# Performance work log

Measured on AMD Instinct MI355X. Metric: run time of the kernel, lower is better.

Reference implementation:

```python
import jax, jax.numpy as jnp
import numpy as np

E = 1024      # embed_dim
H = 16        # num_heads
DH = E // H   # head_dim
CD = 512      # context_dim
S = 2048      # source length
B = 16        # batch
SCALE = DH ** -0.5


def setup_inputs() -> dict:
    key0 = jax.random.key(0)
    ks = jax.random.split(key0, 12)
    inp = {
        "query": jax.random.normal(ks[0], (1, B, E), jnp.float32),
        "key": jax.random.normal(ks[1], (S, B, E), jnp.float32),
        "value": jax.random.normal(ks[2], (S, B, E), jnp.float32),
        "context": jax.random.normal(ks[3], (B, CD), jnp.float32),
        # packed QKV input projection: [3E, E] (rows 0:E -> Q, E:2E -> K, 2E:3E -> V)
        "in_proj_weight": jax.random.normal(ks[4], (3 * E, E), jnp.float32) * 0.02,
        "in_proj_bias": jnp.zeros((3 * E,), jnp.float32),
        # context_layer: Linear(context_dim + embed_dim, embed_dim)
        "ctx_weight": jax.random.normal(ks[5], (E, CD + E), jnp.float32) * 0.02,
        "ctx_bias": jnp.zeros((E,), jnp.float32),
        # out_proj: Linear(E, E)
        "out_weight": jax.random.normal(ks[6], (E, E), jnp.float32) * 0.02,
        "out_bias": jnp.zeros((E,), jnp.float32),
        # bias_k / bias_v: learned extra KV position, shape [1,1,E] in torch
        "bias_k": jax.random.normal(ks[7], (E,), jnp.float32) * 0.02,
        "bias_v": jax.random.normal(ks[8], (E,), jnp.float32) * 0.02,
    }
    return inp


def _attention(query, key, value, context, in_proj_weight, in_proj_bias,
               ctx_weight, ctx_bias, out_weight, out_bias, bias_k, bias_v):
    tgt_len, bsz, _ = query.shape  # tgt_len == 1 (context cat requires it)
    # separate q/k/v input projections (slices of packed weight)
    q = query @ in_proj_weight[:E].T + in_proj_bias[:E]
    k = key @ in_proj_weight[E:2 * E].T + in_proj_bias[E:2 * E]
    v = value @ in_proj_weight[2 * E:].T + in_proj_bias[2 * E:]
    # context injection: concat context along feature dim, project back to E
    ctx_q = context[None]                                # [1, B, CD]
    ctx_k = jnp.broadcast_to(context[None], (k.shape[0], bsz, CD))
    q = jnp.concatenate([ctx_q, q], axis=-1) @ ctx_weight.T + ctx_bias
    k = jnp.concatenate([ctx_k, k], axis=-1) @ ctx_weight.T + ctx_bias
    q = q * SCALE
    # bias_k / bias_v appended as extra source position
    k = jnp.concatenate([k, jnp.broadcast_to(bias_k, (1, bsz, E))], axis=0)
    v = jnp.concatenate([v, jnp.broadcast_to(bias_v, (1, bsz, E))], axis=0)
    src_len = k.shape[0]
    # [L, B, E] -> [B*H, L, DH]
    qh = q.reshape(tgt_len, bsz * H, DH).transpose(1, 0, 2)
    kh = k.reshape(src_len, bsz * H, DH).transpose(1, 0, 2)
    vh = v.reshape(src_len, bsz * H, DH).transpose(1, 0, 2)
    scores = jnp.einsum("btd,bsd->bts", qh, kh)          # [B*H, T, S+1]
    weights = jax.nn.softmax(scores, axis=-1)
    attn = jnp.einsum("bts,bsd->btd", weights, vh)       # [B*H, T, DH]
    attn = attn.transpose(1, 0, 2).reshape(tgt_len, bsz, E)
    attn = attn @ out_weight.T + out_bias
    avg_weights = weights.reshape(bsz, H, tgt_len, src_len).sum(axis=1) / H
    return attn, avg_weights


def reference(query, key, value, context, in_proj_weight, in_proj_bias,
              ctx_weight, ctx_bias, out_weight, out_bias, bias_k, bias_v):
    return _attention(query, key, value, context, in_proj_weight, in_proj_bias,
                      ctx_weight, ctx_bias, out_weight, out_bias, bias_k, bias_v)
```

## Files before the change

### kernel.cpp

```cpp
#include <hip/hip_runtime.h>
#include <math.h>

#define E   1024
#define H   16
#define DH  64
#define CD  512
#define S   2048
#define B   16
#define SRC (S + 1)
#define SPAD 2052
#define SCALE 0.125f

#define OFF_CTXP 0
#define OFF_Q0   16384
#define OFF_BKP  32768
#define OFF_Q1S  33792
#define OFF_CK   50176
#define OFF_TT   66560
#define OFF_C0   328704
#define OFF_GP   328960
#define OFF_SC   1377536
#define OFF_WT   1902848
#define OFF_UP   2427392
#define OFF_U    6621696
#define OFF_AP   6883840

__global__ __launch_bounds__(256) void k_pre1(
    const float* __restrict__ query, const float* __restrict__ context,
    const float* __restrict__ ipw, const float* __restrict__ ipb,
    const float* __restrict__ cw, const float* __restrict__ cb,
    float* __restrict__ ws)
{
    int b  = blockIdx.x >> 6;
    int et = blockIdx.x & 63;
    int grp = threadIdx.x >> 4, l = threadIdx.x & 15;
    int e = et * 16 + grp;
    const float* crow = cw + (size_t)e * (CD + E);
    const float* ctx  = context + b * CD;
    float a1 = 0.f;
    #pragma unroll
    for (int c = l * 4; c < CD; c += 64) {
        float4 w4 = *(const float4*)(crow + c);
        float4 x4 = *(const float4*)(ctx + c);
        a1 += w4.x*x4.x + w4.y*x4.y + w4.z*x4.z + w4.w*x4.w;
    }
    const float* qrow = query + b * E;
    const float* wrow = ipw + (size_t)e * E;
    float a2 = 0.f;
    #pragma unroll
    for (int f = l * 4; f < E; f += 64) {
        float4 w4 = *(const float4*)(wrow + f);
        float4 x4 = *(const float4*)(qrow + f);
        a2 += w4.x*x4.x + w4.y*x4.y + w4.z*x4.z + w4.w*x4.w;
    }
    float a3 = 0.f;
    if (b == 0) {
        const float* c2 = crow + CD;
        const float* bk = ipb + E;
        #pragma unroll
        for (int f = l * 4; f < E; f += 64) {
            float4 w4 = *(const float4*)(c2 + f);
            float4 x4 = *(const float4*)(bk + f);
            a3 += w4.x*x4.x + w4.y*x4.y + w4.z*x4.z + w4.w*x4.w;
        }
    }
    #pragma unroll
    for (int m = 8; m >= 1; m >>= 1) {
        a1 += __shfl_xor(a1, m, 64);
        a2 += __shfl_xor(a2, m, 64);
        a3 += __shfl_xor(a3, m, 64);
    }
    if (l == 0) {
        ws[OFF_CTXP + b*E + e] = a1 + cb[e];
        ws[OFF_Q0   + b*E + e] = a2 + ipb[e];
        if (b == 0) ws[OFF_BKP + e] = a3;
    }
}

__global__ __launch_bounds__(256) void k_pre2(
    const float* __restrict__ cw, float* __restrict__ ws)
{
    int b  = blockIdx.x >> 6;
    int et = blockIdx.x & 63;
    int grp = threadIdx.x >> 4, l = threadIdx.x & 15;
    int e = et * 16 + grp;
    const float* q0 = ws + OFF_Q0 + b*E;
    const float* c2row = cw + (size_t)e * (CD + E) + CD;
    float acc = 0.f;
    #pragma unroll
    for (int f = l * 4; f < E; f += 64) {
        float4 w4 = *(const float4*)(c2row + f);
        float4 x4 = *(const float4*)(q0 + f);
        acc += w4.x*x4.x + w4.y*x4.y + w4.z*x4.z + w4.w*x4.w;
    }
    #pragma unroll
    for (int m = 8; m >= 1; m >>= 1) acc += __shfl_xor(acc, m, 64);
    if (l == 0) {
        float ctxp = ws[OFF_CTXP + b*E + e];
        ws[OFF_Q1S + b*E + e] = (ctxp + acc) * SCALE;
        ws[OFF_CK  + b*E + e] = ctxp + ws[OFF_BKP + e];
    }
}

__global__ __launch_bounds__(256) void k_pre3(
    const float* __restrict__ cw, float* __restrict__ ws)
{
    int bh = blockIdx.x >> 2;
    int f  = ((blockIdx.x & 3) << 8) + threadIdx.x;
    int b = bh >> 4, h = bh & 15;
    const float* q1 = ws + OFF_Q1S + b*E + h*DH;
    float acc = 0.f;
    #pragma unroll 8
    for (int d = 0; d < DH; ++d)
        acc += q1[d] * cw[(size_t)(h*DH + d)*(CD+E) + CD + f];
    ws[OFF_TT + f*256 + bh] = acc;
}

__global__ __launch_bounds__(256) void k_pre3b(
    const float* __restrict__ bias_k, float* __restrict__ ws)
{
    int bh = threadIdx.x;
    int b = bh >> 4, h = bh & 15;
    const float* q1 = ws + OFF_Q1S + b*E + h*DH;
    const float* ck = ws + OFF_CK  + b*E + h*DH;
    const float* bk = bias_k + h*DH;
    float c0 = 0.f, sb = 0.f;
    for (int d = 0; d < DH; ++d) { float q = q1[d]; c0 += q*ck[d]; sb += q*bk[d]; }
    ws[OFF_C0 + bh] = c0;
    ws[OFF_SC + (size_t)bh*SPAD + S] = sb;
}

__global__ __launch_bounds__(256) void k_g(
    const float* __restrict__ ipw, float* __restrict__ ws)
{
    int kc = blockIdx.x >> 7;
    int nt = (blockIdx.x >> 5) & 3;
    int mt = blockIdx.x & 31;
    int n  = (nt << 8) + threadIdx.x;
    int m0 = mt << 3;
    int f0 = kc << 8;
    const float* tT = ws + OFF_TT;
    const float* wk = ipw + (size_t)E * E;
    float acc[8];
    #pragma unroll
    for (int m = 0; m < 8; ++m) acc[m] = 0.f;
    #pragma unroll 4
    for (int f = f0; f < f0 + 256; ++f) {
        float wv = wk[(size_t)f*E + n];
        const float* tr = tT + f*256 + m0;
        #pragma unroll
        for (int m = 0; m < 8; ++m) acc[m] += tr[m] * wv;
    }
    float* gp = ws + OFF_GP + (size_t)kc * (256*E);
    #pragma unroll
    for (int m = 0; m < 8; ++m) gp[(size_t)(m0+m)*E + n] = acc[m];
}

__global__ __launch_bounds__(256) void k_gsum(float* __restrict__ ws)
{
    int id = blockIdx.x * 256 + threadIdx.x;
    float a = ws[OFF_GP + id]
            + ws[OFF_GP + 1*(256*E) + id]
            + ws[OFF_GP + 2*(256*E) + id]
            + ws[OFF_GP + 3*(256*E) + id];
    ws[OFF_GP + id] = a;
}

__global__ __launch_bounds__(512, 2) void k_scores(
    const float* __restrict__ key, float* __restrict__ ws)
{
    __shared__ float lds[8704];
    int b  = blockIdx.x >> 5;
    int sc = blockIdx.x & 31;
    int tid = threadIdx.x;
    int w = __builtin_amdgcn_readfirstlane(tid >> 6);
    int l = tid & 63;
    int r = sc*64 + l;
    const float* kbase = key + (((size_t)r*B + b) << 10) + w*128;
    const float* gbase = ws + OFF_GP + (size_t)b*(16*1024) + w*128;
    float acc[16];
    #pragma unroll
    for (int h = 0; h < 16; ++h) acc[h] = 0.f;

    #pragma unroll 1
    for (int sub = 0; sub < 4; ++sub) {
        const float* kp = kbase + sub*32;
        float4 kk[8];
        #pragma unroll
        for (int j = 0; j < 8; ++j) kk[j] = *(const float4*)(kp + j*4);
        const float* gp0 = gbase + sub*32;
        #pragma unroll
        for (int h = 0; h < 16; ++h) {
            const float* gp = gp0 + h*1024;
            float a = 0.f;
            #pragma unroll
            for (int j = 0; j < 8; ++j) {
                float4 gv = *(const float4*)(gp + j*4);
                a += kk[j].x*gv.x + kk[j].y*gv.y + kk[j].z*gv.z + kk[j].w*gv.w;
            }
            acc[h] += a;
        }
    }

    float* pr = lds + (w*64 + l)*17;
    #pragma unroll
    for (int h = 0; h < 16; ++h) pr[h] = acc[h];
    __syncthreads();

    int l2 = tid & 63, pp = tid >> 6;
    #pragma unroll
    for (int k2 = 0; k2 < 2; ++k2) {
        int h = pp*2 + k2;
        float sum = 0.f;
        #pragma unroll
        for (int ww = 0; ww < 8; ++ww) sum += lds[(ww*64 + l2)*17 + h];
        int bh = b*16 + h;
        ws[OFF_SC + (size_t)bh*SPAD + sc*64 + l2] = sum + ws[OFF_C0 + bh];
    }
}

__global__ __launch_bounds__(256) void k_softmax(float* __restrict__ ws)
{
    int bh = blockIdx.x; int b = bh >> 4, h = bh & 15;
    int tid = threadIdx.x, lane = tid & 63, wid = tid >> 6;
    const float* row = ws + OFF_SC + (size_t)bh*SPAD;
    __shared__ float red[4];
    float v[9];
    float m = -1e30f;
    #pragma unroll
    for (int i = 0; i < 9; ++i) {
        int s = tid + (i << 8);
        if (s < SRC) { v[i] = row[s]; m = fmaxf(m, v[i]); } else v[i] = -1e30f;
    }
    #pragma unroll
    for (int k = 1; k < 64; k <<= 1) m = fmaxf(m, __shfl_xor(m, k, 64));
    if (lane == 0) red[wid] = m;
    __syncthreads();
    m = fmaxf(fmaxf(red[0], red[1]), fmaxf(red[2], red[3]));
    __syncthreads();
    float sum = 0.f;
    #pragma unroll
    for (int i = 0; i < 9; ++i) {
        int s = tid + (i << 8);
        if (s < SRC) { v[i] = expf(v[i] - m); sum += v[i]; }
    }
    #pragma unroll
    for (int k = 1; k < 64; k <<= 1) sum += __shfl_xor(sum, k, 64);
    if (lane == 0) red[wid] = sum;
    __syncthreads();
    sum = red[0] + red[1] + red[2] + red[3];
    float inv = 1.0f / sum;
    float* wt = ws + OFF_WT;
    #pragma unroll
    for (int i = 0; i < 9; ++i) {
        int s = tid + (i << 8);
        if (s < SRC) wt[((size_t)(b*SRC + s) << 4) + h] = v[i] * inv;
    }
}

__global__ __launch_bounds__(256) void k_avg(
    const float* __restrict__ ws, float* __restrict__ out)
{
    int id = blockIdx.x * 256 + threadIdx.x;
    if (id >= B * SRC) return;
    const float* p = ws + OFF_WT + (size_t)id * 16;
    float a = 0.f;
    #pragma unroll
    for (int j = 0; j < 16; j += 4) {
        float4 w4 = *(const float4*)(p + j);
        a += w4.x + w4.y + w4.z + w4.w;
    }
    out[B*E + id] = a * (1.0f / H);
}

__global__ __launch_bounds__(256) void k_u(
    const float* __restrict__ value, float* __restrict__ ws)
{
    int b  = blockIdx.x >> 5;
    int sc = (blockIdx.x >> 1) & 15;
    int fh = blockIdx.x & 1;
    int f  = (fh << 9) + threadIdx.x * 2;
    float2 acc[16];
    #pragma unroll
    for (int h = 0; h < 16; ++h) { acc[h].x = 0.f; acc[h].y = 0.f; }
    int s0 = sc << 7;
    for (int i = 0; i < 128; ++i) {
        int s = s0 + i;
        const float* wr = ws + OFF_WT + ((size_t)(b*SRC + s) << 4);
        float2 vv = *(const float2*)(value + (((size_t)s*B + b) << 10) + f);
        #pragma unroll
        for (int h = 0; h < 16; ++h) {
            float wv = wr[h];
            acc[h].x += wv * vv.x; acc[h].y += wv * vv.y;
        }
    }
    float* up = ws + OFF_UP + ((size_t)(sc*B + b) << 4) * E;
    #pragma unroll
    for (int h = 0; h < 16; ++h)
        *(float2*)(up + (size_t)h*E + f) = acc[h];
}

__global__ __launch_bounds__(256) void k_ured(float* __restrict__ ws)
{
    int id = blockIdx.x * 256 + threadIdx.x;
    float a = 0.f;
    #pragma unroll
    for (int c = 0; c < 16; ++c) a += ws[OFF_UP + (size_t)c*(B*H*E) + id];
    ws[OFF_U + id] = a;
}

__global__ __launch_bounds__(256) void k_attnpre(
    const float* __restrict__ ipw, const float* __restrict__ ipb,
    const float* __restrict__ bias_v, float* __restrict__ ws)
{
    int b  = blockIdx.x >> 6;
    int et = blockIdx.x & 63;
    int grp = threadIdx.x >> 4, l = threadIdx.x & 15;
    int e = et * 16 + grp;
    int h = e >> 6;
    const float* wvr = ipw + (size_t)(2*E + e) * E;
    const float* ur  = ws + OFF_U + (size_t)(b*16 + h) * E;
    float acc = 0.f;
    #pragma unroll
    for (int ff = l * 4; ff < E; ff += 64) {
        float4 w4 = *(const float4*)(wvr + ff);
        float4 u4 = *(const float4*)(ur + ff);
        acc += w4.x*u4.x + w4.y*u4.y + w4.z*u4.z + w4.w*u4.w;
    }
    #pragma unroll
    for (int m = 8; m >= 1; m >>= 1) acc += __shfl_xor(acc, m, 64);
    if (l == 0) {
        float wS = ws[OFF_WT + ((size_t)(b*SRC + S) << 4) + h];
        ws[OFF_AP + b*E + e] = acc + ipb[2*E + e] * (1.0f - wS) + wS * bias_v[e];
    }
}

__global__ __launch_bounds__(256) void k_out(
    const float* __restrict__ ow, const float* __restrict__ ob,
    const float* __restrict__ ws, float* __restrict__ out)
{
    int b  = blockIdx.x >> 6;
    int et = blockIdx.x & 63;
    int grp = threadIdx.x >> 4, l = threadIdx.x & 15;
    int o = et * 16 + grp;
    const float* wr = ow + (size_t)o * E;
    const float* ap = ws + OFF_AP + b*E;
    float acc = 0.f;
    #pragma unroll
    for (int e = l * 4; e < E; e += 64) {
        float4 w4 = *(const float4*)(wr + e);
        float4 a4 = *(const float4*)(ap + e);
        acc += w4.x*a4.x + w4.y*a4.y + w4.z*a4.z + w4.w*a4.w;
    }
    #pragma unroll
    for (int m = 8; m >= 1; m >>= 1) acc += __shfl_xor(acc, m, 64);
    if (l == 0) out[b*E + o] = acc + ob[o];
}

extern "C" void kernel_launch(void* const* d_in, const int* in_sizes, int n_in,
                              void* d_out, int out_size, void* d_ws, size_t ws_size,
                              hipStream_t stream)
{
    const float* query   = (const float*)d_in[0];
    const float* key     = (const float*)d_in[1];
    const float* value   = (const float*)d_in[2];
    const float* context = (const float*)d_in[3];
    const float* ipw     = (const float*)d_in[4];
    const float* ipb     = (const float*)d_in[5];
    const float* cw      = (const float*)d_in[6];
    const float* cb      = (const float*)d_in[7];
    const float* ow      = (const float*)d_in[8];
    const float* ob      = (const float*)d_in[9];
    const float* bias_k  = (const float*)d_in[10];
    const float* bias_v  = (const float*)d_in[11];
    float* out = (float*)d_out;
    float* ws  = (float*)d_ws;

    hipLaunchKernelGGL(k_pre1,    dim3(1024), dim3(256),  0, stream, query, context, ipw, ipb, cw, cb, ws);
    hipLaunchKernelGGL(k_pre2,    dim3(1024), dim3(256),  0, stream, cw, ws);
    hipLaunchKernelGGL(k_pre3,    dim3(1024), dim3(256),  0, stream, cw, ws);
    hipLaunchKernelGGL(k_pre3b,   dim3(1),    dim3(256),  0, stream, bias_k, ws);
    hipLaunchKernelGGL(k_g,       dim3(512),  dim3(256),  0, stream, ipw, ws);
    hipLaunchKernelGGL(k_gsum,    dim3(1024), dim3(256),  0, stream, ws);
    hipLaunchKernelGGL(k_scores,  dim3(512),  dim3(512),  0, stream, key, ws);
    hipLaunchKernelGGL(k_softmax, dim3(256),  dim3(256),  0, stream, ws);
    hipLaunchKernelGGL(k_avg,     dim3(129),  dim3(256),  0, stream, ws, out);
    hipLaunchKernelGGL(k_u,       dim3(512),  dim3(256),  0, stream, value, ws);
    hipLaunchKernelGGL(k_ured,    dim3(1024), dim3(256),  0, stream, ws);
    hipLaunchKernelGGL(k_attnpre, dim3(1024), dim3(256),  0, stream, ipw, ipb, bias_v, ws);
    hipLaunchKernelGGL(k_out,     dim3(1024), dim3(256),  0, stream, ow, ob, ws, out);
}
```

Baseline: 193.3 us.

## Transpose weight/T layouts, fold pre3b into scores, drop U reduction kernel

Switches the softmax-weight buffer from [b,s,h] to a per-head row layout [bh,s] and the T buffer to [bh,f], so writes are coalesced and pre3 uses float4 loads over fewer blocks. The tiny single-block pre3b kernel is removed: each scores block recomputes the c0 and bias_k terms in shared memory. k_u now processes 64 source rows per block with float4 values, and the separate 16-way reduction kernel is removed; k_attnpre instead loops over 32 partial U chunks, with the W_v row held in registers. This cuts two launches and improves access patterns, but attnpre now reads much more partial data and k_g reads T with a 1024 stride.

```diff
diff --git a/kernel.cpp b/kernel.cpp
--- a/kernel.cpp
+++ b/kernel.cpp
@@ -17,13 +17,11 @@
 #define OFF_Q1S  33792
 #define OFF_CK   50176
 #define OFF_TT   66560
-#define OFF_C0   328704
 #define OFF_GP   328960
 #define OFF_SC   1377536
 #define OFF_WT   1902848
 #define OFF_UP   2427392
-#define OFF_U    6621696
-#define OFF_AP   6883840
+#define OFF_AP   10816000
 
 __global__ __launch_bounds__(256) void k_pre1(
     const float* __restrict__ query, const float* __restrict__ context,
@@ -105,29 +103,18 @@
 __global__ __launch_bounds__(256) void k_pre3(
     const float* __restrict__ cw, float* __restrict__ ws)
 {
-    int bh = blockIdx.x >> 2;
-    int f  = ((blockIdx.x & 3) << 8) + threadIdx.x;
+    int bh = blockIdx.x;
     int b = bh >> 4, h = bh & 15;
+    int f = threadIdx.x * 4;
     const float* q1 = ws + OFF_Q1S + b*E + h*DH;
-    float acc = 0.f;
+    float4 a; a.x = a.y = a.z = a.w = 0.f;
     #pragma unroll 8
-    for (int d = 0; d < DH; ++d)
-        acc += q1[d] * cw[(size_t)(h*DH + d)*(CD+E) + CD + f];
-    ws[OFF_TT + f*256 + bh] = acc;
-}
-
-__global__ __launch_bounds__(256) void k_pre3b(
-    const float* __restrict__ bias_k, float* __restrict__ ws)
-{
-    int bh = threadIdx.x;
-    int b = bh >> 4, h = bh & 15;
-    const float* q1 = ws + OFF_Q1S + b*E + h*DH;
-    const float* ck = ws + OFF_CK  + b*E + h*DH;
-    const float* bk = bias_k + h*DH;
-    float c0 = 0.f, sb = 0.f;
-    for (int d = 0; d < DH; ++d) { float q = q1[d]; c0 += q*ck[d]; sb += q*bk[d]; }
-    ws[OFF_C0 + bh] = c0;
-    ws[OFF_SC + (size_t)bh*SPAD + S] = sb;
+    for (int d = 0; d < DH; ++d) {
+        float q = q1[d];
+        float4 w4 = *(const float4*)(cw + (size_t)(h*DH + d)*(CD+E) + CD + f);
+        a.x += q*w4.x; a.y += q*w4.y; a.z += q*w4.z; a.w += q*w4.w;
+    }
+    *(float4*)(ws + OFF_TT + (size_t)bh*1024 + f) = a;
 }
 
 __global__ __launch_bounds__(256) void k_g(
@@ -147,9 +134,9 @@
     #pragma unroll 4
     for (int f = f0; f < f0 + 256; ++f) {
         float wv = wk[(size_t)f*E + n];
-        const float* tr = tT + f*256 + m0;
-        #pragma unroll
-        for (int m = 0; m < 8; ++m) acc[m] += tr[m] * wv;
+        #pragma unroll
+        for (int m = 0; m < 8; ++m)
+            acc[m] += tT[(size_t)(m0+m)*1024 + f] * wv;
     }
     float* gp = ws + OFF_GP + (size_t)kc * (256*E);
     #pragma unroll
@@ -167,12 +154,28 @@
 }
 
 __global__ __launch_bounds__(512, 2) void k_scores(
-    const float* __restrict__ key, float* __restrict__ ws)
+    const float* __restrict__ key, const float* __restrict__ bias_k,
+    float* __restrict__ ws)
 {
     __shared__ float lds[8704];
+    __shared__ float exA[256];
+    __shared__ float exB[256];
     int b  = blockIdx.x >> 5;
     int sc = blockIdx.x & 31;
     int tid = threadIdx.x;
+
+    if (tid < 256) {
+        int h = tid >> 4, seg = tid & 15;
+        const float* q1 = ws + OFF_Q1S + b*E + h*DH + seg*4;
+        const float* ck = ws + OFF_CK  + b*E + h*DH + seg*4;
+        const float* bk = bias_k + h*DH + seg*4;
+        float4 q4 = *(const float4*)q1;
+        float4 c4 = *(const float4*)ck;
+        float4 b4 = *(const float4*)bk;
+        exA[tid] = q4.x*c4.x + q4.y*c4.y + q4.z*c4.z + q4.w*c4.w;
+        exB[tid] = q4.x*b4.x + q4.y*b4.y + q4.z*b4.z + q4.w*b4.w;
+    }
+
     int w = __builtin_amdgcn_readfirstlane(tid >> 6);
     int l = tid & 63;
     int r = sc*64 + l;
@@ -214,14 +217,23 @@
         float sum = 0.f;
         #pragma unroll
         for (int ww = 0; ww < 8; ++ww) sum += lds[(ww*64 + l2)*17 + h];
+        float c0 = 0.f;
+        #pragma unroll
+        for (int seg = 0; seg < 16; ++seg) c0 += exA[h*16 + seg];
         int bh = b*16 + h;
-        ws[OFF_SC + (size_t)bh*SPAD + sc*64 + l2] = sum + ws[OFF_C0 + bh];
+        ws[OFF_SC + (size_t)bh*SPAD + sc*64 + l2] = sum + c0;
+        if (sc == 0 && l2 == 0) {
+            float sb = 0.f;
+            #pragma unroll
+            for (int seg = 0; seg < 16; ++seg) sb += exB[h*16 + seg];
+            ws[OFF_SC + (size_t)bh*SPAD + S] = sb;
+        }
     }
 }
 
 __global__ __launch_bounds__(256) void k_softmax(float* __restrict__ ws)
 {
-    int bh = blockIdx.x; int b = bh >> 4, h = bh & 15;
+    int bh = blockIdx.x;
     int tid = threadIdx.x, lane = tid & 63, wid = tid >> 6;
     const float* row = ws + OFF_SC + (size_t)bh*SPAD;
     __shared__ float red[4];
@@ -250,63 +262,60 @@
     __syncthreads();
     sum = red[0] + red[1] + red[2] + red[3];
     float inv = 1.0f / sum;
-    float* wt = ws + OFF_WT;
+    float* wrow = ws + OFF_WT + (size_t)bh*SRC;
     #pragma unroll
     for (int i = 0; i < 9; ++i) {
         int s = tid + (i << 8);
-        if (s < SRC) wt[((size_t)(b*SRC + s) << 4) + h] = v[i] * inv;
+        if (s < SRC) wrow[s] = v[i] * inv;
     }
 }
 
 __global__ __launch_bounds__(256) void k_avg(
     const float* __restrict__ ws, float* __restrict__ out)
 {
-    int id = blockIdx.x * 256 + threadIdx.x;
-    if (id >= B * SRC) return;
-    const float* p = ws + OFF_WT + (size_t)id * 16;
+    int b = blockIdx.x / 9, i = blockIdx.x % 9;
+    int s = i*256 + threadIdx.x;
+    if (s >= SRC) return;
+    const float* p = ws + OFF_WT + (size_t)(b*16)*SRC + s;
     float a = 0.f;
     #pragma unroll
-    for (int j = 0; j < 16; j += 4) {
-        float4 w4 = *(const float4*)(p + j);
-        a += w4.x + w4.y + w4.z + w4.w;
-    }
-    out[B*E + id] = a * (1.0f / H);
+    for (int h = 0; h < 16; ++h) a += p[(size_t)h*SRC];
+    out[B*E + b*SRC + s] = a * (1.0f / H);
 }
 
 __global__ __launch_bounds__(256) void k_u(
     const float* __restrict__ value, float* __restrict__ ws)
 {
     int b  = blockIdx.x >> 5;
-    int sc = (blockIdx.x >> 1) & 15;
-    int fh = blockIdx.x & 1;
-    int f  = (fh << 9) + threadIdx.x * 2;
-    float2 acc[16];
-    #pragma unroll
-    for (int h = 0; h < 16; ++h) { acc[h].x = 0.f; acc[h].y = 0.f; }
-    int s0 = sc << 7;
-    for (int i = 0; i < 128; ++i) {
-        int s = s0 + i;
-        const float* wr = ws + OFF_WT + ((size_t)(b*SRC + s) << 4);
-        float2 vv = *(const float2*)(value + (((size_t)s*B + b) << 10) + f);
+    int sc = blockIdx.x & 31;
+    int f  = threadIdx.x * 4;
+    const float* wtb = ws + OFF_WT + (size_t)(b*16)*SRC;
+    float4 acc[16];
+    #pragma unroll
+    for (int h = 0; h < 16; ++h) { acc[h].x = acc[h].y = acc[h].z = acc[h].w = 0.f; }
+    int s0 = sc * 64;
+    #pragma unroll 1
+    for (int sub = 0; sub < 8; ++sub) {
+        int ss = s0 + sub*8;
+        float4 vv[8];
+        #pragma unroll
+        for (int j = 0; j < 8; ++j)
+            vv[j] = *(const float4*)(value + (((size_t)(ss+j)*B + b) << 10) + f);
         #pragma unroll
         for (int h = 0; h < 16; ++h) {
-            float wv = wr[h];
-            acc[h].x += wv * vv.x; acc[h].y += wv * vv.y;
+            const float* wr = wtb + (size_t)h*SRC + ss;
+            #pragma unroll
+            for (int j = 0; j < 8; ++j) {
+                float wv = wr[j];
+                acc[h].x += wv*vv[j].x; acc[h].y += wv*vv[j].y;
+                acc[h].z += wv*vv[j].z; acc[h].w += wv*vv[j].w;
+            }
         }
     }
-    float* up = ws + OFF_UP + ((size_t)(sc*B + b) << 4) * E;
+    float* up = ws + OFF_UP + ((size_t)(sc*B + b)*16)*1024;
     #pragma unroll
     for (int h = 0; h < 16; ++h)
-        *(float2*)(up + (size_t)h*E + f) = acc[h];
-}
-
-__global__ __launch_bounds__(256) void k_ured(float* __restrict__ ws)
-{
-    int id = blockIdx.x * 256 + threadIdx.x;
-    float a = 0.f;
-    #pragma unroll
-    for (int c = 0; c < 16; ++c) a += ws[OFF_UP + (size_t)c*(B*H*E) + id];
-    ws[OFF_U + id] = a;
+        *(float4*)(up + (size_t)h*1024 + f) = acc[h];
 }
 
 __global__ __launch_bounds__(256) void k_attnpre(
@@ -319,18 +328,24 @@
     int e = et * 16 + grp;
     int h = e >> 6;
     const float* wvr = ipw + (size_t)(2*E + e) * E;
-    const float* ur  = ws + OFF_U + (size_t)(b*16 + h) * E;
+    float4 wv[16];
+    #pragma unroll
+    for (int i = 0; i < 16; ++i)
+        wv[i] = *(const float4*)(wvr + l*4 + i*64);
     float acc = 0.f;
-    #pragma unroll
-    for (int ff = l * 4; ff < E; ff += 64) {
-        float4 w4 = *(const float4*)(wvr + ff);
-        float4 u4 = *(const float4*)(ur + ff);
-        acc += w4.x*u4.x + w4.y*u4.y + w4.z*u4.z + w4.w*u4.w;
+    #pragma unroll 1
+    for (int sc = 0; sc < 32; ++sc) {
+        const float* ur = ws + OFF_UP + ((size_t)((sc*B + b)*16 + h))*1024;
+        #pragma unroll
+        for (int i = 0; i < 16; ++i) {
+            float4 u4 = *(const float4*)(ur + l*4 + i*64);
+            acc += wv[i].x*u4.x + wv[i].y*u4.y + wv[i].z*u4.z + wv[i].w*u4.w;
+        }
     }
     #pragma unroll
     for (int m = 8; m >= 1; m >>= 1) acc += __shfl_xor(acc, m, 64);
     if (l == 0) {
-        float wS = ws[OFF_WT + ((size_t)(b*SRC + S) << 4) + h];
+        float wS = ws[OFF_WT + (size_t)(b*16 + h)*SRC + S];
         ws[OFF_AP + b*E + e] = acc + ipb[2*E + e] * (1.0f - wS) + wS * bias_v[e];
     }
 }
@@ -378,15 +393,13 @@
 
     hipLaunchKernelGGL(k_pre1,    dim3(1024), dim3(256),  0, stream, query, context, ipw, ipb, cw, cb, ws);
     hipLaunchKernelGGL(k_pre2,    dim3(1024), dim3(256),  0, stream, cw, ws);
-    hipLaunchKernelGGL(k_pre3,    dim3(1024), dim3(256),  0, stream, cw, ws);
-    hipLaunchKernelGGL(k_pre3b,   dim3(1),    dim3(256),  0, stream, bias_k, ws);
+    hipLaunchKernelGGL(k_pre3,    dim3(256),  dim3(256),  0, stream, cw, ws);
     hipLaunchKernelGGL(k_g,       dim3(512),  dim3(256),  0, stream, ipw, ws);
     hipLaunchKernelGGL(k_gsum,    dim3(1024), dim3(256),  0, stream, ws);
-    hipLaunchKernelGGL(k_scores,  dim3(512),  dim3(512),  0, stream, key, ws);
+    hipLaunchKernelGGL(k_scores,  dim3(512),  dim3(512),  0, stream, key, bias_k, ws);
     hipLaunchKernelGGL(k_softmax, dim3(256),  dim3(256),  0, stream, ws);
-    hipLaunchKernelGGL(k_avg,     dim3(129),  dim3(256),  0, stream, ws, out);
+    hipLaunchKernelGGL(k_avg,     dim3(144),  dim3(256),  0, stream, ws, out);
     hipLaunchKernelGGL(k_u,       dim3(512),  dim3(256),  0, stream, value, ws);
-    hipLaunchKernelGGL(k_ured,    dim3(1024), dim3(256),  0, stream, ws);
     hipLaunchKernelGGL(k_attnpre, dim3(1024), dim3(256),  0, stream, ipw, ipb, bias_v, ws);
     hipLaunchKernelGGL(k_out,     dim3(1024), dim3(256),  0, stream, ow, ob, ws, out);
 }
```

After: 251.4 us. 30.1% more time.
